# Optimization experiments

Hardware: AMD Instinct MI355X
Metric: run time of the kernel (lower is better)

Reference implementation:

```python
import jax, jax.numpy as jnp
import numpy as np

EMB_DIM = 16
NUM_EXPERTS = 8
TOPK = 2
HIDDEN = 4 * EMB_DIM  # assumed Expert hidden width


def setup_inputs() -> dict:
    key = jax.random.key(0)
    ks = jax.random.split(key, 8)
    B, S = 64, 4096
    s = 1.0 / np.sqrt(EMB_DIM)
    sh = 1.0 / np.sqrt(HIDDEN)
    return {
        "x": jax.random.normal(ks[0], (B, S, EMB_DIM), jnp.float32),
        "Wr": jax.random.uniform(ks[1], (EMB_DIM, NUM_EXPERTS), jnp.float32, -s, s),
        "br": jax.random.uniform(ks[2], (NUM_EXPERTS,), jnp.float32, -s, s),
        "W1": jax.random.uniform(ks[3], (NUM_EXPERTS, EMB_DIM, HIDDEN), jnp.float32, -s, s),
        "b1": jax.random.uniform(ks[4], (NUM_EXPERTS, HIDDEN), jnp.float32, -s, s),
        "W2": jax.random.uniform(ks[5], (NUM_EXPERTS, HIDDEN, EMB_DIM), jnp.float32, -sh, sh),
        "b2": jax.random.uniform(ks[6], (NUM_EXPERTS, EMB_DIM), jnp.float32, -sh, sh),
    }


def reference(x, Wr, br, W1, b1, W2, b2):
    # Router: softmax gate over all experts, then top-k expert selection.
    gate = jax.nn.softmax(x @ Wr + br, axis=-1)            # [B,S,E]
    _, topk_idx = jax.lax.top_k(gate, TOPK)                 # [B,S,TOPK]

    moe_out = jnp.zeros_like(x)
    # Small fixed loop over experts (mirrors the module's expert loop).
    for i in range(NUM_EXPERTS):
        sel = (topk_idx == i).any(axis=-1)                  # [B,S] bool
        w = gate[..., i] * sel                              # masked gate score
        h = jax.nn.relu(x @ W1[i] + b1[i])                  # [B,S,HIDDEN]
        eo = h @ W2[i] + b2[i]                              # [B,S,EMB_DIM]
        moe_out = moe_out + eo * w[..., None]
    return moe_out
```

## Files before the change

kernel.cpp:

```cpp
#include <hip/hip_runtime.h>
#include <hip/hip_bf16.h>

#define EMB 16
#define HID 64
#define NE  8
#define TPG 64

typedef float  f32x4 __attribute__((ext_vector_type(4)));
typedef double f64x4 __attribute__((ext_vector_type(4)));
typedef short  s16x4 __attribute__((ext_vector_type(4)));

__device__ __forceinline__ short f2bf(float f) {
    union { __hip_bfloat16 h; short s; } u;
    u.h = __float2bfloat16(f);
    return u.s;
}
__device__ __forceinline__ s16x4 pack_bf16x4(float a, float b, float c, float d) {
    s16x4 r;
    r[0] = f2bf(a); r[1] = f2bf(b); r[2] = f2bf(c); r[3] = f2bf(d);
    return r;
}

__device__ __forceinline__ f32x4 vfmaf(float s, f32x4 a, f32x4 c) {
    f32x4 r;
    r[0] = fmaf(s, a[0], c[0]); r[1] = fmaf(s, a[1], c[1]);
    r[2] = fmaf(s, a[2], c[2]); r[3] = fmaf(s, a[3], c[3]);
    return r;
}
__device__ __forceinline__ f64x4 vfmad(double s, f32x4 a, f64x4 c) {
    f64x4 r;
    r[0] = fma(s, (double)a[0], c[0]); r[1] = fma(s, (double)a[1], c[1]);
    r[2] = fma(s, (double)a[2], c[2]); r[3] = fma(s, (double)a[3], c[3]);
    return r;
}

__global__ __launch_bounds__(256, 2)
void router_k(const float* __restrict__ x, const float* __restrict__ Wr,
              const float* __restrict__ br, float* __restrict__ gates,
              int n_tokens)
{
    __shared__ float wr_lds[EMB * NE];
    __shared__ float br_lds[NE];
    const int tid = threadIdx.x;
    if (tid < EMB * NE) wr_lds[tid] = Wr[tid];
    if (tid < NE) br_lds[tid] = br[tid];
    __syncthreads();

    const int t = blockIdx.x * 256 + tid;
    if (t >= n_tokens) return;

    const f32x4* xp = (const f32x4*)(x + (size_t)t * EMB);
    const f32x4 x0 = xp[0], x1 = xp[1], x2 = xp[2], x3 = xp[3];

    f32x4 lgA = *(const f32x4*)(br_lds + 0);
    f32x4 lgB = *(const f32x4*)(br_lds + 4);
#define RSTEP(K, XV) do { const float xv_ = (XV); \
        lgA = vfmaf(xv_, *(const f32x4*)(wr_lds + (K) * NE),     lgA); \
        lgB = vfmaf(xv_, *(const f32x4*)(wr_lds + (K) * NE + 4), lgB); } while (0)
    RSTEP(0,  x0[0]); RSTEP(1,  x0[1]); RSTEP(2,  x0[2]); RSTEP(3,  x0[3]);
    RSTEP(4,  x1[0]); RSTEP(5,  x1[1]); RSTEP(6,  x1[2]); RSTEP(7,  x1[3]);
    RSTEP(8,  x2[0]); RSTEP(9,  x2[1]); RSTEP(10, x2[2]); RSTEP(11, x2[3]);
    RSTEP(12, x3[0]); RSTEP(13, x3[1]); RSTEP(14, x3[2]); RSTEP(15, x3[3]);
#undef RSTEP

    float m1 = -1e30f, m2 = -1e30f, m3 = -1e30f;
#define MSCAN(V) do { const float v_ = (V); \
        const float hi_ = fmaxf(m1, v_), lo_ = fminf(m1, v_); \
        const float hi2_ = fmaxf(m2, lo_), lo2_ = fminf(m2, lo_); \
        m1 = hi_; m2 = hi2_; m3 = fmaxf(m3, lo2_); } while (0)
    MSCAN(lgA[0]); MSCAN(lgA[1]); MSCAN(lgA[2]); MSCAN(lgA[3]);
    MSCAN(lgB[0]); MSCAN(lgB[1]); MSCAN(lgB[2]); MSCAN(lgB[3]);
#undef MSCAN

    int sm = 0;
    sm |= (lgA[0] >= m2) << 0; sm |= (lgA[1] >= m2) << 1;
    sm |= (lgA[2] >= m2) << 2; sm |= (lgA[3] >= m2) << 3;
    sm |= (lgB[0] >= m2) << 4; sm |= (lgB[1] >= m2) << 5;
    sm |= (lgB[2] >= m2) << 6; sm |= (lgB[3] >= m2) << 7;

    if (__any(m2 - m3 < 1e-4f)) {
        f64x4 dA, dB;
        dA[0] = (double)br_lds[0]; dA[1] = (double)br_lds[1];
        dA[2] = (double)br_lds[2]; dA[3] = (double)br_lds[3];
        dB[0] = (double)br_lds[4]; dB[1] = (double)br_lds[5];
        dB[2] = (double)br_lds[6]; dB[3] = (double)br_lds[7];
#define DSTEP(K, XV) do { const double xv_ = (double)(XV); \
        dA = vfmad(xv_, *(const f32x4*)(wr_lds + (K) * NE),     dA); \
        dB = vfmad(xv_, *(const f32x4*)(wr_lds + (K) * NE + 4), dB); } while (0)
        DSTEP(0,  x0[0]); DSTEP(1,  x0[1]); DSTEP(2,  x0[2]); DSTEP(3,  x0[3]);
        DSTEP(4,  x1[0]); DSTEP(5,  x1[1]); DSTEP(6,  x1[2]); DSTEP(7,  x1[3]);
        DSTEP(8,  x2[0]); DSTEP(9,  x2[1]); DSTEP(10, x2[2]); DSTEP(11, x2[3]);
        DSTEP(12, x3[0]); DSTEP(13, x3[1]); DSTEP(14, x3[2]); DSTEP(15, x3[3]);
#undef DSTEP
        double M1 = -1e300, M2 = -1e300;
#define DSCAN(V) do { const double v_ = (V); \
        const double hi_ = fmax(M1, v_); M2 = fmax(M2, fmin(M1, v_)); M1 = hi_; } while (0)
        DSCAN(dA[0]); DSCAN(dA[1]); DSCAN(dA[2]); DSCAN(dA[3]);
        DSCAN(dB[0]); DSCAN(dB[1]); DSCAN(dB[2]); DSCAN(dB[3]);
#undef DSCAN
        sm = 0;
        sm |= (dA[0] >= M2) << 0; sm |= (dA[1] >= M2) << 1;
        sm |= (dA[2] >= M2) << 2; sm |= (dA[3] >= M2) << 3;
        sm |= (dB[0] >= M2) << 4; sm |= (dB[1] >= M2) << 5;
        sm |= (dB[2] >= M2) << 6; sm |= (dB[3] >= M2) << 7;
    }

    const float e0 = __expf(lgA[0] - m1), e1 = __expf(lgA[1] - m1);
    const float e2 = __expf(lgA[2] - m1), e3 = __expf(lgA[3] - m1);
    const float e4 = __expf(lgB[0] - m1), e5 = __expf(lgB[1] - m1);
    const float e6 = __expf(lgB[2] - m1), e7 = __expf(lgB[3] - m1);
    const float inv = 1.0f / (e0 + e1 + e2 + e3 + e4 + e5 + e6 + e7);
    f32x4 gA, gB;
    gA[0] = (sm & 1)   ? e0 * inv : 0.f;  gA[1] = (sm & 2)   ? e1 * inv : 0.f;
    gA[2] = (sm & 4)   ? e2 * inv : 0.f;  gA[3] = (sm & 8)   ? e3 * inv : 0.f;
    gB[0] = (sm & 16)  ? e4 * inv : 0.f;  gB[1] = (sm & 32)  ? e5 * inv : 0.f;
    gB[2] = (sm & 64)  ? e6 * inv : 0.f;  gB[3] = (sm & 128) ? e7 * inv : 0.f;

    f32x4* gp = (f32x4*)(gates + (size_t)t * NE);
    gp[0] = gA;
    gp[1] = gB;
}

__global__ __launch_bounds__(256, 2)
void moe_k(const float* __restrict__ x, const float* __restrict__ gates,
           const float* __restrict__ W1, const float* __restrict__ b1,
           const float* __restrict__ W2, const float* __restrict__ b2,
           float* __restrict__ out, int n_tokens)
{
    __shared__ __align__(16) s16x4 w1lds[NE * 4 * 64];
    __shared__ __align__(16) s16x4 w2lds[NE * 4 * 64];
    __shared__ __align__(16) float b1_lds[NE * HID];
    __shared__ __align__(16) float b2_lds[NE * EMB];
    __shared__ __align__(16) float wt_lds[4 * 8 * TPG];

    const int tid = threadIdx.x;

    for (int s = tid; s < NE * 4 * 64; s += 256) {
        const int e = s >> 8, nq = (s >> 6) & 3, l = s & 63;
        const int cc = l & 15, gg = (l >> 4) & 3;
        const float* w1p = W1 + (e * EMB + 4 * gg) * HID + 16 * nq + cc;
        const float* w2p = W2 + (e * HID + 16 * nq + 4 * gg) * EMB + cc;
        w1lds[s] = pack_bf16x4(w1p[0], w1p[HID], w1p[2 * HID], w1p[3 * HID]);
        w2lds[s] = pack_bf16x4(w2p[0], w2p[EMB], w2p[2 * EMB], w2p[3 * EMB]);
    }
    for (int i = tid; i < NE * HID; i += 256) b1_lds[i] = b1[i];
    if (tid < NE * EMB) b2_lds[tid] = b2[tid];
    __syncthreads();

    const int lane = tid & 63;
    const int wid  = tid >> 6;
    const int col  = lane & 15;
    const int cg   = lane >> 4;
    float* wtw = wt_lds + wid * (NE * TPG);

    const int n_groups = n_tokens / TPG;
    for (int g = blockIdx.x * 4 + wid; g < n_groups; g += gridDim.x * 4) {
        const int tok0 = g * TPG;

        {
            const f32x4* gp = (const f32x4*)(gates + (size_t)(tok0 + lane) * NE);
            const f32x4 ga = gp[0], gb = gp[1];
#pragma unroll
            for (int e = 0; e < 4; ++e) wtw[e * TPG + lane] = ga[e];
#pragma unroll
            for (int e = 4; e < 8; ++e) wtw[e * TPG + lane] = gb[e - 4];
        }

        s16x4 xb0, xb1, xb2, xb3;
        {
            const f32x4 v0 = *(const f32x4*)(x + (size_t)(tok0 +  0 + col) * EMB + 4 * cg);
            const f32x4 v1 = *(const f32x4*)(x + (size_t)(tok0 + 16 + col) * EMB + 4 * cg);
            const f32x4 v2 = *(const f32x4*)(x + (size_t)(tok0 + 32 + col) * EMB + 4 * cg);
            const f32x4 v3 = *(const f32x4*)(x + (size_t)(tok0 + 48 + col) * EMB + 4 * cg);
            xb0 = pack_bf16x4(v0[0], v0[1], v0[2], v0[3]);
            xb1 = pack_bf16x4(v1[0], v1[1], v1[2], v1[3]);
            xb2 = pack_bf16x4(v2[0], v2[1], v2[2], v2[3]);
            xb3 = pack_bf16x4(v3[0], v3[1], v3[2], v3[3]);
        }

        f32x4 oacc0 = {0.f,0.f,0.f,0.f}, oacc1 = {0.f,0.f,0.f,0.f};
        f32x4 oacc2 = {0.f,0.f,0.f,0.f}, oacc3 = {0.f,0.f,0.f,0.f};

#pragma unroll 1
        for (int e = 0; e < NE; ++e) {
            const float wv0 = wtw[e * TPG +  0 + col];
            const float wv1 = wtw[e * TPG + 16 + col];
            const float wv2 = wtw[e * TPG + 32 + col];
            const float wv3 = wtw[e * TPG + 48 + col];

            f32x4 h0[4], h1[4], h2[4], h3[4];
#pragma unroll
            for (int n = 0; n < 4; ++n) {
                const s16x4 a1  = w1lds[(e * 4 + n) * 64 + lane];
                const f32x4 b1c = *(const f32x4*)(b1_lds + e * HID + 16 * n + 4 * cg);
                h0[n] = __builtin_amdgcn_mfma_f32_16x16x16bf16_1k(a1, xb0, b1c, 0, 0, 0);
                h1[n] = __builtin_amdgcn_mfma_f32_16x16x16bf16_1k(a1, xb1, b1c, 0, 0, 0);
                h2[n] = __builtin_amdgcn_mfma_f32_16x16x16bf16_1k(a1, xb2, b1c, 0, 0, 0);
                h3[n] = __builtin_amdgcn_mfma_f32_16x16x16bf16_1k(a1, xb3, b1c, 0, 0, 0);
            }

            const f32x4 b2c = *(const f32x4*)(b2_lds + e * EMB + 4 * cg);
            f32x4 eo0 = b2c, eo1 = b2c, eo2 = b2c, eo3 = b2c;
#pragma unroll
            for (int q = 0; q < 4; ++q) {
                const s16x4 a2 = w2lds[(e * 4 + q) * 64 + lane];
                const s16x4 p0 = pack_bf16x4(fmaxf(h0[q][0], 0.f), fmaxf(h0[q][1], 0.f),
                                             fmaxf(h0[q][2], 0.f), fmaxf(h0[q][3], 0.f));
                const s16x4 p1 = pack_bf16x4(fmaxf(h1[q][0], 0.f), fmaxf(h1[q][1], 0.f),
                                             fmaxf(h1[q][2], 0.f), fmaxf(h1[q][3], 0.f));
                const s16x4 p2 = pack_bf16x4(fmaxf(h2[q][0], 0.f), fmaxf(h2[q][1], 0.f),
                                             fmaxf(h2[q][2], 0.f), fmaxf(h2[q][3], 0.f));
                const s16x4 p3 = pack_bf16x4(fmaxf(h3[q][0], 0.f), fmaxf(h3[q][1], 0.f),
                                             fmaxf(h3[q][2], 0.f), fmaxf(h3[q][3], 0.f));
                eo0 = __builtin_amdgcn_mfma_f32_16x16x16bf16_1k(a2, p0, eo0, 0, 0, 0);
                eo1 = __builtin_amdgcn_mfma_f32_16x16x16bf16_1k(a2, p1, eo1, 0, 0, 0);
                eo2 = __builtin_amdgcn_mfma_f32_16x16x16bf16_1k(a2, p2, eo2, 0, 0, 0);
                eo3 = __builtin_amdgcn_mfma_f32_16x16x16bf16_1k(a2, p3, eo3, 0, 0, 0);
            }

            oacc0 = vfmaf(wv0, eo0, oacc0);
            oacc1 = vfmaf(wv1, eo1, oacc1);
            oacc2 = vfmaf(wv2, eo2, oacc2);
            oacc3 = vfmaf(wv3, eo3, oacc3);
        }

        *(f32x4*)(out + (size_t)(tok0 +  0 + col) * EMB + 4 * cg) = oacc0;
        *(f32x4*)(out + (size_t)(tok0 + 16 + col) * EMB + 4 * cg) = oacc1;
        *(f32x4*)(out + (size_t)(tok0 + 32 + col) * EMB + 4 * cg) = oacc2;
        *(f32x4*)(out + (size_t)(tok0 + 48 + col) * EMB + 4 * cg) = oacc3;
    }
}

extern "C" void kernel_launch(void* const* d_in, const int* in_sizes, int n_in,
                              void* d_out, int out_size, void* d_ws, size_t ws_size,
                              hipStream_t stream) {
    const float* x  = (const float*)d_in[0];
    const float* Wr = (const float*)d_in[1];
    const float* br = (const float*)d_in[2];
    const float* W1 = (const float*)d_in[3];
    const float* b1 = (const float*)d_in[4];
    const float* W2 = (const float*)d_in[5];
    const float* b2 = (const float*)d_in[6];
    float* out = (float*)d_out;

    const int n_tokens = in_sizes[0] / EMB;
    float* gates = (float*)d_ws;

    hipLaunchKernelGGL(router_k, dim3((n_tokens + 255) / 256), dim3(256), 0, stream,
                       x, Wr, br, gates, n_tokens);
    hipLaunchKernelGGL(moe_k, dim3(1024), dim3(256), 0, stream,
                       x, gates, W1, b1, W2, b2, out, n_tokens);
}
```

Measured before the change: 34.83 us.

## Fuse router into MoE kernel using split-bf16 MFMA for gate logits

Drops the separate router kernel and its gates buffer. Router logits are now computed inside the MoE kernel with three bf16 MFMAs that split weights and inputs into hi/lo parts, then softmax and top-2 run per token using lane shuffles. If any token in the wave has a near-tie, the gates for the whole group are recomputed in fp64. This removes one kernel launch and the gates write/read round trip, at the cost of extra MFMA and shuffle work plus some wave-divergent fallback in the main kernel.

```diff
diff --git a/kernel.cpp b/kernel.cpp
--- a/kernel.cpp
+++ b/kernel.cpp
@@ -15,12 +15,16 @@
     u.h = __float2bfloat16(f);
     return u.s;
 }
+__device__ __forceinline__ float bf2f(short s) {
+    union { unsigned u; float f; } v;
+    v.u = ((unsigned)(unsigned short)s) << 16;
+    return v.f;
+}
 __device__ __forceinline__ s16x4 pack_bf16x4(float a, float b, float c, float d) {
     s16x4 r;
     r[0] = f2bf(a); r[1] = f2bf(b); r[2] = f2bf(c); r[3] = f2bf(d);
     return r;
 }
-
 __device__ __forceinline__ f32x4 vfmaf(float s, f32x4 a, f32x4 c) {
     f32x4 r;
     r[0] = fmaf(s, a[0], c[0]); r[1] = fmaf(s, a[1], c[1]);
@@ -35,103 +39,19 @@
 }
 
 __global__ __launch_bounds__(256, 2)
-void router_k(const float* __restrict__ x, const float* __restrict__ Wr,
-              const float* __restrict__ br, float* __restrict__ gates,
-              int n_tokens)
-{
-    __shared__ float wr_lds[EMB * NE];
-    __shared__ float br_lds[NE];
-    const int tid = threadIdx.x;
-    if (tid < EMB * NE) wr_lds[tid] = Wr[tid];
-    if (tid < NE) br_lds[tid] = br[tid];
-    __syncthreads();
-
-    const int t = blockIdx.x * 256 + tid;
-    if (t >= n_tokens) return;
-
-    const f32x4* xp = (const f32x4*)(x + (size_t)t * EMB);
-    const f32x4 x0 = xp[0], x1 = xp[1], x2 = xp[2], x3 = xp[3];
-
-    f32x4 lgA = *(const f32x4*)(br_lds + 0);
-    f32x4 lgB = *(const f32x4*)(br_lds + 4);
-#define RSTEP(K, XV) do { const float xv_ = (XV); \
-        lgA = vfmaf(xv_, *(const f32x4*)(wr_lds + (K) * NE),     lgA); \
-        lgB = vfmaf(xv_, *(const f32x4*)(wr_lds + (K) * NE + 4), lgB); } while (0)
-    RSTEP(0,  x0[0]); RSTEP(1,  x0[1]); RSTEP(2,  x0[2]); RSTEP(3,  x0[3]);
-    RSTEP(4,  x1[0]); RSTEP(5,  x1[1]); RSTEP(6,  x1[2]); RSTEP(7,  x1[3]);
-    RSTEP(8,  x2[0]); RSTEP(9,  x2[1]); RSTEP(10, x2[2]); RSTEP(11, x2[3]);
-    RSTEP(12, x3[0]); RSTEP(13, x3[1]); RSTEP(14, x3[2]); RSTEP(15, x3[3]);
-#undef RSTEP
-
-    float m1 = -1e30f, m2 = -1e30f, m3 = -1e30f;
-#define MSCAN(V) do { const float v_ = (V); \
-        const float hi_ = fmaxf(m1, v_), lo_ = fminf(m1, v_); \
-        const float hi2_ = fmaxf(m2, lo_), lo2_ = fminf(m2, lo_); \
-        m1 = hi_; m2 = hi2_; m3 = fmaxf(m3, lo2_); } while (0)
-    MSCAN(lgA[0]); MSCAN(lgA[1]); MSCAN(lgA[2]); MSCAN(lgA[3]);
-    MSCAN(lgB[0]); MSCAN(lgB[1]); MSCAN(lgB[2]); MSCAN(lgB[3]);
-#undef MSCAN
-
-    int sm = 0;
-    sm |= (lgA[0] >= m2) << 0; sm |= (lgA[1] >= m2) << 1;
-    sm |= (lgA[2] >= m2) << 2; sm |= (lgA[3] >= m2) << 3;
-    sm |= (lgB[0] >= m2) << 4; sm |= (lgB[1] >= m2) << 5;
-    sm |= (lgB[2] >= m2) << 6; sm |= (lgB[3] >= m2) << 7;
-
-    if (__any(m2 - m3 < 1e-4f)) {
-        f64x4 dA, dB;
-        dA[0] = (double)br_lds[0]; dA[1] = (double)br_lds[1];
-        dA[2] = (double)br_lds[2]; dA[3] = (double)br_lds[3];
-        dB[0] = (double)br_lds[4]; dB[1] = (double)br_lds[5];
-        dB[2] = (double)br_lds[6]; dB[3] = (double)br_lds[7];
-#define DSTEP(K, XV) do { const double xv_ = (double)(XV); \
-        dA = vfmad(xv_, *(const f32x4*)(wr_lds + (K) * NE),     dA); \
-        dB = vfmad(xv_, *(const f32x4*)(wr_lds + (K) * NE + 4), dB); } while (0)
-        DSTEP(0,  x0[0]); DSTEP(1,  x0[1]); DSTEP(2,  x0[2]); DSTEP(3,  x0[3]);
-        DSTEP(4,  x1[0]); DSTEP(5,  x1[1]); DSTEP(6,  x1[2]); DSTEP(7,  x1[3]);
-        DSTEP(8,  x2[0]); DSTEP(9,  x2[1]); DSTEP(10, x2[2]); DSTEP(11, x2[3]);
-        DSTEP(12, x3[0]); DSTEP(13, x3[1]); DSTEP(14, x3[2]); DSTEP(15, x3[3]);
-#undef DSTEP
-        double M1 = -1e300, M2 = -1e300;
-#define DSCAN(V) do { const double v_ = (V); \
-        const double hi_ = fmax(M1, v_); M2 = fmax(M2, fmin(M1, v_)); M1 = hi_; } while (0)
-        DSCAN(dA[0]); DSCAN(dA[1]); DSCAN(dA[2]); DSCAN(dA[3]);
-        DSCAN(dB[0]); DSCAN(dB[1]); DSCAN(dB[2]); DSCAN(dB[3]);
-#undef DSCAN
-        sm = 0;
-        sm |= (dA[0] >= M2) << 0; sm |= (dA[1] >= M2) << 1;
-        sm |= (dA[2] >= M2) << 2; sm |= (dA[3] >= M2) << 3;
-        sm |= (dB[0] >= M2) << 4; sm |= (dB[1] >= M2) << 5;
-        sm |= (dB[2] >= M2) << 6; sm |= (dB[3] >= M2) << 7;
-    }
-
-    const float e0 = __expf(lgA[0] - m1), e1 = __expf(lgA[1] - m1);
-    const float e2 = __expf(lgA[2] - m1), e3 = __expf(lgA[3] - m1);
-    const float e4 = __expf(lgB[0] - m1), e5 = __expf(lgB[1] - m1);
-    const float e6 = __expf(lgB[2] - m1), e7 = __expf(lgB[3] - m1);
-    const float inv = 1.0f / (e0 + e1 + e2 + e3 + e4 + e5 + e6 + e7);
-    f32x4 gA, gB;
-    gA[0] = (sm & 1)   ? e0 * inv : 0.f;  gA[1] = (sm & 2)   ? e1 * inv : 0.f;
-    gA[2] = (sm & 4)   ? e2 * inv : 0.f;  gA[3] = (sm & 8)   ? e3 * inv : 0.f;
-    gB[0] = (sm & 16)  ? e4 * inv : 0.f;  gB[1] = (sm & 32)  ? e5 * inv : 0.f;
-    gB[2] = (sm & 64)  ? e6 * inv : 0.f;  gB[3] = (sm & 128) ? e7 * inv : 0.f;
-
-    f32x4* gp = (f32x4*)(gates + (size_t)t * NE);
-    gp[0] = gA;
-    gp[1] = gB;
-}
-
-__global__ __launch_bounds__(256, 2)
-void moe_k(const float* __restrict__ x, const float* __restrict__ gates,
-           const float* __restrict__ W1, const float* __restrict__ b1,
-           const float* __restrict__ W2, const float* __restrict__ b2,
-           float* __restrict__ out, int n_tokens)
+void moe_all(const float* __restrict__ x, const float* __restrict__ Wr,
+             const float* __restrict__ br, const float* __restrict__ W1,
+             const float* __restrict__ b1, const float* __restrict__ W2,
+             const float* __restrict__ b2, float* __restrict__ out,
+             int n_tokens)
 {
     __shared__ __align__(16) s16x4 w1lds[NE * 4 * 64];
     __shared__ __align__(16) s16x4 w2lds[NE * 4 * 64];
     __shared__ __align__(16) float b1_lds[NE * HID];
     __shared__ __align__(16) float b2_lds[NE * EMB];
-    __shared__ __align__(16) float wt_lds[4 * 8 * TPG];
+    __shared__ __align__(16) float wr_lds[EMB * NE];
+    __shared__ __align__(16) float br_lds[NE];
+    __shared__ __align__(16) float wt_lds[4 * NE * TPG];
 
     const int tid = threadIdx.x;
 
@@ -145,6 +65,8 @@
     }
     for (int i = tid; i < NE * HID; i += 256) b1_lds[i] = b1[i];
     if (tid < NE * EMB) b2_lds[tid] = b2[tid];
+    if (tid < EMB * NE) wr_lds[tid] = Wr[tid];
+    if (tid < NE) br_lds[tid] = br[tid];
     __syncthreads();
 
     const int lane = tid & 63;
@@ -153,31 +75,96 @@
     const int cg   = lane >> 4;
     float* wtw = wt_lds + wid * (NE * TPG);
 
+    s16x4 wra_hi, wra_lo;
+    f32x4 brc;
+#pragma unroll
+    for (int j = 0; j < 4; ++j) {
+        const float wv = (col < NE) ? wr_lds[(4 * cg + j) * NE + col] : 0.f;
+        const short hi = f2bf(wv);
+        wra_hi[j] = hi;
+        wra_lo[j] = f2bf(wv - bf2f(hi));
+    }
+#pragma unroll
+    for (int r = 0; r < 4; ++r) brc[r] = br_lds[(4 * cg + r) & (NE - 1)];
+
     const int n_groups = n_tokens / TPG;
     for (int g = blockIdx.x * 4 + wid; g < n_groups; g += gridDim.x * 4) {
         const int tok0 = g * TPG;
-
-        {
-            const f32x4* gp = (const f32x4*)(gates + (size_t)(tok0 + lane) * NE);
-            const f32x4 ga = gp[0], gb = gp[1];
-#pragma unroll
-            for (int e = 0; e < 4; ++e) wtw[e * TPG + lane] = ga[e];
-#pragma unroll
-            for (int e = 4; e < 8; ++e) wtw[e * TPG + lane] = gb[e - 4];
+        bool tie = false;
+        s16x4 xbT[4];
+
+#pragma unroll
+        for (int T = 0; T < 4; ++T) {
+            const f32x4 xv = *(const f32x4*)(x + (size_t)(tok0 + 16 * T + col) * EMB + 4 * cg);
+            const s16x4 xh = pack_bf16x4(xv[0], xv[1], xv[2], xv[3]);
+            const s16x4 xl = pack_bf16x4(xv[0] - bf2f(xh[0]), xv[1] - bf2f(xh[1]),
+                                         xv[2] - bf2f(xh[2]), xv[3] - bf2f(xh[3]));
+            xbT[T] = xh;
+            f32x4 lg = __builtin_amdgcn_mfma_f32_16x16x16bf16_1k(wra_hi, xh, brc, 0, 0, 0);
+            lg = __builtin_amdgcn_mfma_f32_16x16x16bf16_1k(wra_hi, xl, lg, 0, 0, 0);
+            lg = __builtin_amdgcn_mfma_f32_16x16x16bf16_1k(wra_lo, xh, lg, 0, 0, 0);
+            float ot0 = __shfl_xor(lg[0], 16, 64), ot1 = __shfl_xor(lg[1], 16, 64);
+            float ot2 = __shfl_xor(lg[2], 16, 64), ot3 = __shfl_xor(lg[3], 16, 64);
+            float m1 = -1e30f, m2 = -1e30f, m3 = -1e30f;
+#define MSCAN(V) do { const float v_ = (V); \
+        const float hi_ = fmaxf(m1, v_), lo_ = fminf(m1, v_); \
+        const float hi2_ = fmaxf(m2, lo_), lo2_ = fminf(m2, lo_); \
+        m1 = hi_; m2 = hi2_; m3 = fmaxf(m3, lo2_); } while (0)
+            MSCAN(lg[0]); MSCAN(lg[1]); MSCAN(lg[2]); MSCAN(lg[3]);
+            MSCAN(ot0);   MSCAN(ot1);   MSCAN(ot2);   MSCAN(ot3);
+#undef MSCAN
+            const float e0 = __expf(lg[0] - m1), e1 = __expf(lg[1] - m1);
+            const float e2 = __expf(lg[2] - m1), e3 = __expf(lg[3] - m1);
+            const float f0 = __expf(ot0 - m1),   f1 = __expf(ot1 - m1);
+            const float f2 = __expf(ot2 - m1),   f3 = __expf(ot3 - m1);
+            const float inv = 1.0f / (e0 + e1 + e2 + e3 + f0 + f1 + f2 + f3);
+            if (cg < 2) {
+                wtw[(4 * cg + 0) * TPG + 16 * T + col] = (lg[0] >= m2) ? e0 * inv : 0.f;
+                wtw[(4 * cg + 1) * TPG + 16 * T + col] = (lg[1] >= m2) ? e1 * inv : 0.f;
+                wtw[(4 * cg + 2) * TPG + 16 * T + col] = (lg[2] >= m2) ? e2 * inv : 0.f;
+                wtw[(4 * cg + 3) * TPG + 16 * T + col] = (lg[3] >= m2) ? e3 * inv : 0.f;
+                tie = tie || (m2 - m3 < 5e-4f);
+            }
         }
 
-        s16x4 xb0, xb1, xb2, xb3;
-        {
-            const f32x4 v0 = *(const f32x4*)(x + (size_t)(tok0 +  0 + col) * EMB + 4 * cg);
-            const f32x4 v1 = *(const f32x4*)(x + (size_t)(tok0 + 16 + col) * EMB + 4 * cg);
-            const f32x4 v2 = *(const f32x4*)(x + (size_t)(tok0 + 32 + col) * EMB + 4 * cg);
-            const f32x4 v3 = *(const f32x4*)(x + (size_t)(tok0 + 48 + col) * EMB + 4 * cg);
-            xb0 = pack_bf16x4(v0[0], v0[1], v0[2], v0[3]);
-            xb1 = pack_bf16x4(v1[0], v1[1], v1[2], v1[3]);
-            xb2 = pack_bf16x4(v2[0], v2[1], v2[2], v2[3]);
-            xb3 = pack_bf16x4(v3[0], v3[1], v3[2], v3[3]);
+        if (__any(tie)) {
+            const f32x4* xp = (const f32x4*)(x + (size_t)(tok0 + lane) * EMB);
+            const f32x4 x0 = xp[0], x1 = xp[1], x2 = xp[2], x3 = xp[3];
+            f64x4 dA, dB;
+            dA[0] = (double)br_lds[0]; dA[1] = (double)br_lds[1];
+            dA[2] = (double)br_lds[2]; dA[3] = (double)br_lds[3];
+            dB[0] = (double)br_lds[4]; dB[1] = (double)br_lds[5];
+            dB[2] = (double)br_lds[6]; dB[3] = (double)br_lds[7];
+#define DSTEP(K, XV) do { const double xv_ = (double)(XV); \
+        dA = vfmad(xv_, *(const f32x4*)(wr_lds + (K) * NE),     dA); \
+        dB = vfmad(xv_, *(const f32x4*)(wr_lds + (K) * NE + 4), dB); } while (0)
+            DSTEP(0,  x0[0]); DSTEP(1,  x0[1]); DSTEP(2,  x0[2]); DSTEP(3,  x0[3]);
+            DSTEP(4,  x1[0]); DSTEP(5,  x1[1]); DSTEP(6,  x1[2]); DSTEP(7,  x1[3]);
+            DSTEP(8,  x2[0]); DSTEP(9,  x2[1]); DSTEP(10, x2[2]); DSTEP(11, x2[3]);
+            DSTEP(12, x3[0]); DSTEP(13, x3[1]); DSTEP(14, x3[2]); DSTEP(15, x3[3]);
+#undef DSTEP
+            double M1 = -1e300, M2 = -1e300;
+#define DSCAN(V) do { const double v_ = (V); \
+        const double hi_ = fmax(M1, v_); M2 = fmax(M2, fmin(M1, v_)); M1 = hi_; } while (0)
+            DSCAN(dA[0]); DSCAN(dA[1]); DSCAN(dA[2]); DSCAN(dA[3]);
+            DSCAN(dB[0]); DSCAN(dB[1]); DSCAN(dB[2]); DSCAN(dB[3]);
+#undef DSCAN
+            const float g0 = __expf((float)(dA[0] - M1)), g1 = __expf((float)(dA[1] - M1));
+            const float g2 = __expf((float)(dA[2] - M1)), g3 = __expf((float)(dA[3] - M1));
+            const float g4 = __expf((float)(dB[0] - M1)), g5 = __expf((float)(dB[1] - M1));
+            const float g6 = __expf((float)(dB[2] - M1)), g7 = __expf((float)(dB[3] - M1));
+            const float inv = 1.0f / (g0 + g1 + g2 + g3 + g4 + g5 + g6 + g7);
+            wtw[0 * TPG + lane] = (dA[0] >= M2) ? g0 * inv : 0.f;
+            wtw[1 * TPG + lane] = (dA[1] >= M2) ? g1 * inv : 0.f;
+            wtw[2 * TPG + lane] = (dA[2] >= M2) ? g2 * inv : 0.f;
+            wtw[3 * TPG + lane] = (dA[3] >= M2) ? g3 * inv : 0.f;
+            wtw[4 * TPG + lane] = (dB[0] >= M2) ? g4 * inv : 0.f;
+            wtw[5 * TPG + lane] = (dB[1] >= M2) ? g5 * inv : 0.f;
+            wtw[6 * TPG + lane] = (dB[2] >= M2) ? g6 * inv : 0.f;
+            wtw[7 * TPG + lane] = (dB[3] >= M2) ? g7 * inv : 0.f;
         }
 
+        const s16x4 xb0 = xbT[0], xb1 = xbT[1], xb2 = xbT[2], xb3 = xbT[3];
         f32x4 oacc0 = {0.f,0.f,0.f,0.f}, oacc1 = {0.f,0.f,0.f,0.f};
         f32x4 oacc2 = {0.f,0.f,0.f,0.f}, oacc3 = {0.f,0.f,0.f,0.f};
 
@@ -244,10 +231,6 @@
     float* out = (float*)d_out;
 
     const int n_tokens = in_sizes[0] / EMB;
-    float* gates = (float*)d_ws;
-
-    hipLaunchKernelGGL(router_k, dim3((n_tokens + 255) / 256), dim3(256), 0, stream,
-                       x, Wr, br, gates, n_tokens);
-    hipLaunchKernelGGL(moe_k, dim3(1024), dim3(256), 0, stream,
-                       x, gates, W1, b1, W2, b2, out, n_tokens);
-}
+    hipLaunchKernelGGL(moe_all, dim3(1024), dim3(256), 0, stream,
+                       x, Wr, br, W1, b1, W2, b2, out, n_tokens);
+}
```

Result: slower. 81.19 us (+133.1%).

## Process two token groups per wave and halve grid to amortize weight staging

Applied to the files above, without the earlier changes.

Each wave now handles two 64-token groups, loading each expert's W1/W2 fragments and biases from LDS once per expert and reusing them for both groups. The grid is halved so each block stages the bf16 weight tables into LDS for twice as many tokens, and the grid-stride loop is replaced with a single assignment per wave. This raises register pressure and assumes the grid exactly covers all token pairs.

```diff
diff --git a/kernel.cpp b/kernel.cpp
--- a/kernel.cpp
+++ b/kernel.cpp
@@ -131,7 +131,7 @@
     __shared__ __align__(16) s16x4 w2lds[NE * 4 * 64];
     __shared__ __align__(16) float b1_lds[NE * HID];
     __shared__ __align__(16) float b2_lds[NE * EMB];
-    __shared__ __align__(16) float wt_lds[4 * 8 * TPG];
+    __shared__ __align__(16) float wt_lds[4 * 2 * NE * TPG];
 
     const int tid = threadIdx.x;
 
@@ -151,59 +151,82 @@
     const int wid  = tid >> 6;
     const int col  = lane & 15;
     const int cg   = lane >> 4;
-    float* wtw = wt_lds + wid * (NE * TPG);
-
-    const int n_groups = n_tokens / TPG;
-    for (int g = blockIdx.x * 4 + wid; g < n_groups; g += gridDim.x * 4) {
-        const int tok0 = g * TPG;
+    float* wtw = wt_lds + wid * (2 * NE * TPG);
+
+    const int n_pairs = n_tokens / (2 * TPG);
+    const int p = blockIdx.x * 4 + wid;
+    if (p >= n_pairs) return;
+    const int tokA0 = p * (2 * TPG);
+    const int tokB0 = tokA0 + TPG;
+
+    {
+        const f32x4* gpA = (const f32x4*)(gates + (size_t)(tokA0 + lane) * NE);
+        const f32x4 ga = gpA[0], gb = gpA[1];
+#pragma unroll
+        for (int e = 0; e < 4; ++e) wtw[e * TPG + lane] = ga[e];
+#pragma unroll
+        for (int e = 4; e < 8; ++e) wtw[e * TPG + lane] = gb[e - 4];
+        const f32x4* gpB = (const f32x4*)(gates + (size_t)(tokB0 + lane) * NE);
+        const f32x4 gc = gpB[0], gd = gpB[1];
+#pragma unroll
+        for (int e = 0; e < 4; ++e) wtw[(NE + e) * TPG + lane] = gc[e];
+#pragma unroll
+        for (int e = 4; e < 8; ++e) wtw[(NE + e) * TPG + lane] = gd[e - 4];
+    }
+
+    s16x4 xa0, xa1, xa2, xa3, xb0, xb1, xb2, xb3;
+    {
+        const f32x4 v0 = *(const f32x4*)(x + (size_t)(tokA0 +  0 + col) * EMB + 4 * cg);
+        const f32x4 v1 = *(const f32x4*)(x + (size_t)(tokA0 + 16 + col) * EMB + 4 * cg);
+        const f32x4 v2 = *(const f32x4*)(x + (size_t)(tokA0 + 32 + col) * EMB + 4 * cg);
+        const f32x4 v3 = *(const f32x4*)(x + (size_t)(tokA0 + 48 + col) * EMB + 4 * cg);
+        xa0 = pack_bf16x4(v0[0], v0[1], v0[2], v0[3]);
+        xa1 = pack_bf16x4(v1[0], v1[1], v1[2], v1[3]);
+        xa2 = pack_bf16x4(v2[0], v2[1], v2[2], v2[3]);
+        xa3 = pack_bf16x4(v3[0], v3[1], v3[2], v3[3]);
+        const f32x4 u0 = *(const f32x4*)(x + (size_t)(tokB0 +  0 + col) * EMB + 4 * cg);
+        const f32x4 u1 = *(const f32x4*)(x + (size_t)(tokB0 + 16 + col) * EMB + 4 * cg);
+        const f32x4 u2 = *(const f32x4*)(x + (size_t)(tokB0 + 32 + col) * EMB + 4 * cg);
+        const f32x4 u3 = *(const f32x4*)(x + (size_t)(tokB0 + 48 + col) * EMB + 4 * cg);
+        xb0 = pack_bf16x4(u0[0], u0[1], u0[2], u0[3]);
+        xb1 = pack_bf16x4(u1[0], u1[1], u1[2], u1[3]);
+        xb2 = pack_bf16x4(u2[0], u2[1], u2[2], u2[3]);
+        xb3 = pack_bf16x4(u3[0], u3[1], u3[2], u3[3]);
+    }
+
+    f32x4 oA0 = {0.f,0.f,0.f,0.f}, oA1 = {0.f,0.f,0.f,0.f};
+    f32x4 oA2 = {0.f,0.f,0.f,0.f}, oA3 = {0.f,0.f,0.f,0.f};
+    f32x4 oB0 = {0.f,0.f,0.f,0.f}, oB1 = {0.f,0.f,0.f,0.f};
+    f32x4 oB2 = {0.f,0.f,0.f,0.f}, oB3 = {0.f,0.f,0.f,0.f};
+
+#pragma unroll 1
+    for (int e = 0; e < NE; ++e) {
+        s16x4 a1f[4], a2f[4];
+        f32x4 b1c[4];
+#pragma unroll
+        for (int n = 0; n < 4; ++n) {
+            a1f[n] = w1lds[(e * 4 + n) * 64 + lane];
+            b1c[n] = *(const f32x4*)(b1_lds + e * HID + 16 * n + 4 * cg);
+            a2f[n] = w2lds[(e * 4 + n) * 64 + lane];
+        }
+        const f32x4 b2c = *(const f32x4*)(b2_lds + e * EMB + 4 * cg);
 
         {
-            const f32x4* gp = (const f32x4*)(gates + (size_t)(tok0 + lane) * NE);
-            const f32x4 ga = gp[0], gb = gp[1];
-#pragma unroll
-            for (int e = 0; e < 4; ++e) wtw[e * TPG + lane] = ga[e];
-#pragma unroll
-            for (int e = 4; e < 8; ++e) wtw[e * TPG + lane] = gb[e - 4];
-        }
-
-        s16x4 xb0, xb1, xb2, xb3;
-        {
-            const f32x4 v0 = *(const f32x4*)(x + (size_t)(tok0 +  0 + col) * EMB + 4 * cg);
-            const f32x4 v1 = *(const f32x4*)(x + (size_t)(tok0 + 16 + col) * EMB + 4 * cg);
-            const f32x4 v2 = *(const f32x4*)(x + (size_t)(tok0 + 32 + col) * EMB + 4 * cg);
-            const f32x4 v3 = *(const f32x4*)(x + (size_t)(tok0 + 48 + col) * EMB + 4 * cg);
-            xb0 = pack_bf16x4(v0[0], v0[1], v0[2], v0[3]);
-            xb1 = pack_bf16x4(v1[0], v1[1], v1[2], v1[3]);
-            xb2 = pack_bf16x4(v2[0], v2[1], v2[2], v2[3]);
-            xb3 = pack_bf16x4(v3[0], v3[1], v3[2], v3[3]);
-        }
-
-        f32x4 oacc0 = {0.f,0.f,0.f,0.f}, oacc1 = {0.f,0.f,0.f,0.f};
-        f32x4 oacc2 = {0.f,0.f,0.f,0.f}, oacc3 = {0.f,0.f,0.f,0.f};
-
-#pragma unroll 1
-        for (int e = 0; e < NE; ++e) {
             const float wv0 = wtw[e * TPG +  0 + col];
             const float wv1 = wtw[e * TPG + 16 + col];
             const float wv2 = wtw[e * TPG + 32 + col];
             const float wv3 = wtw[e * TPG + 48 + col];
-
             f32x4 h0[4], h1[4], h2[4], h3[4];
 #pragma unroll
             for (int n = 0; n < 4; ++n) {
-                const s16x4 a1  = w1lds[(e * 4 + n) * 64 + lane];
-                const f32x4 b1c = *(const f32x4*)(b1_lds + e * HID + 16 * n + 4 * cg);
-                h0[n] = __builtin_amdgcn_mfma_f32_16x16x16bf16_1k(a1, xb0, b1c, 0, 0, 0);
-                h1[n] = __builtin_amdgcn_mfma_f32_16x16x16bf16_1k(a1, xb1, b1c, 0, 0, 0);
-                h2[n] = __builtin_amdgcn_mfma_f32_16x16x16bf16_1k(a1, xb2, b1c, 0, 0, 0);
-                h3[n] = __builtin_amdgcn_mfma_f32_16x16x16bf16_1k(a1, xb3, b1c, 0, 0, 0);
+                h0[n] = __builtin_amdgcn_mfma_f32_16x16x16bf16_1k(a1f[n], xa0, b1c[n], 0, 0, 0);
+                h1[n] = __builtin_amdgcn_mfma_f32_16x16x16bf16_1k(a1f[n], xa1, b1c[n], 0, 0, 0);
+                h2[n] = __builtin_amdgcn_mfma_f32_16x16x16bf16_1k(a1f[n], xa2, b1c[n], 0, 0, 0);
+                h3[n] = __builtin_amdgcn_mfma_f32_16x16x16bf16_1k(a1f[n], xa3, b1c[n], 0, 0, 0);
             }
-
-            const f32x4 b2c = *(const f32x4*)(b2_lds + e * EMB + 4 * cg);
             f32x4 eo0 = b2c, eo1 = b2c, eo2 = b2c, eo3 = b2c;
 #pragma unroll
             for (int q = 0; q < 4; ++q) {
-                const s16x4 a2 = w2lds[(e * 4 + q) * 64 + lane];
                 const s16x4 p0 = pack_bf16x4(fmaxf(h0[q][0], 0.f), fmaxf(h0[q][1], 0.f),
                                              fmaxf(h0[q][2], 0.f), fmaxf(h0[q][3], 0.f));
                 const s16x4 p1 = pack_bf16x4(fmaxf(h1[q][0], 0.f), fmaxf(h1[q][1], 0.f),
@@ -212,23 +235,61 @@
                                              fmaxf(h2[q][2], 0.f), fmaxf(h2[q][3], 0.f));
                 const s16x4 p3 = pack_bf16x4(fmaxf(h3[q][0], 0.f), fmaxf(h3[q][1], 0.f),
                                              fmaxf(h3[q][2], 0.f), fmaxf(h3[q][3], 0.f));
-                eo0 = __builtin_amdgcn_mfma_f32_16x16x16bf16_1k(a2, p0, eo0, 0, 0, 0);
-                eo1 = __builtin_amdgcn_mfma_f32_16x16x16bf16_1k(a2, p1, eo1, 0, 0, 0);
-                eo2 = __builtin_amdgcn_mfma_f32_16x16x16bf16_1k(a2, p2, eo2, 0, 0, 0);
-                eo3 = __builtin_amdgcn_mfma_f32_16x16x16bf16_1k(a2, p3, eo3, 0, 0, 0);
+                eo0 = __builtin_amdgcn_mfma_f32_16x16x16bf16_1k(a2f[q], p0, eo0, 0, 0, 0);
+                eo1 = __builtin_amdgcn_mfma_f32_16x16x16bf16_1k(a2f[q], p1, eo1, 0, 0, 0);
+                eo2 = __builtin_amdgcn_mfma_f32_16x16x16bf16_1k(a2f[q], p2, eo2, 0, 0, 0);
+                eo3 = __builtin_amdgcn_mfma_f32_16x16x16bf16_1k(a2f[q], p3, eo3, 0, 0, 0);
             }
-
-            oacc0 = vfmaf(wv0, eo0, oacc0);
-            oacc1 = vfmaf(wv1, eo1, oacc1);
-            oacc2 = vfmaf(wv2, eo2, oacc2);
-            oacc3 = vfmaf(wv3, eo3, oacc3);
+            oA0 = vfmaf(wv0, eo0, oA0);
+            oA1 = vfmaf(wv1, eo1, oA1);
+            oA2 = vfmaf(wv2, eo2, oA2);
+            oA3 = vfmaf(wv3, eo3, oA3);
         }
 
-        *(f32x4*)(out + (size_t)(tok0 +  0 + col) * EMB + 4 * cg) = oacc0;
-        *(f32x4*)(out + (size_t)(tok0 + 16 + col) * EMB + 4 * cg) = oacc1;
-        *(f32x4*)(out + (size_t)(tok0 + 32 + col) * EMB + 4 * cg) = oacc2;
-        *(f32x4*)(out + (size_t)(tok0 + 48 + col) * EMB + 4 * cg) = oacc3;
-    }
+        {
+            const float wv0 = wtw[(NE + e) * TPG +  0 + col];
+            const float wv1 = wtw[(NE + e) * TPG + 16 + col];
+            const float wv2 = wtw[(NE + e) * TPG + 32 + col];
+            const float wv3 = wtw[(NE + e) * TPG + 48 + col];
+            f32x4 h0[4], h1[4], h2[4], h3[4];
+#pragma unroll
+            for (int n = 0; n < 4; ++n) {
+                h0[n] = __builtin_amdgcn_mfma_f32_16x16x16bf16_1k(a1f[n], xb0, b1c[n], 0, 0, 0);
+                h1[n] = __builtin_amdgcn_mfma_f32_16x16x16bf16_1k(a1f[n], xb1, b1c[n], 0, 0, 0);
+                h2[n] = __builtin_amdgcn_mfma_f32_16x16x16bf16_1k(a1f[n], xb2, b1c[n], 0, 0, 0);
+                h3[n] = __builtin_amdgcn_mfma_f32_16x16x16bf16_1k(a1f[n], xb3, b1c[n], 0, 0, 0);
+            }
+            f32x4 eo0 = b2c, eo1 = b2c, eo2 = b2c, eo3 = b2c;
+#pragma unroll
+            for (int q = 0; q < 4; ++q) {
+                const s16x4 p0 = pack_bf16x4(fmaxf(h0[q][0], 0.f), fmaxf(h0[q][1], 0.f),
+                                             fmaxf(h0[q][2], 0.f), fmaxf(h0[q][3], 0.f));
+                const s16x4 p1 = pack_bf16x4(fmaxf(h1[q][0], 0.f), fmaxf(h1[q][1], 0.f),
+                                             fmaxf(h1[q][2], 0.f), fmaxf(h1[q][3], 0.f));
+                const s16x4 p2 = pack_bf16x4(fmaxf(h2[q][0], 0.f), fmaxf(h2[q][1], 0.f),
+                                             fmaxf(h2[q][2], 0.f), fmaxf(h2[q][3], 0.f));
+                const s16x4 p3 = pack_bf16x4(fmaxf(h3[q][0], 0.f), fmaxf(h3[q][1], 0.f),
+                                             fmaxf(h3[q][2], 0.f), fmaxf(h3[q][3], 0.f));
+                eo0 = __builtin_amdgcn_mfma_f32_16x16x16bf16_1k(a2f[q], p0, eo0, 0, 0, 0);
+                eo1 = __builtin_amdgcn_mfma_f32_16x16x16bf16_1k(a2f[q], p1, eo1, 0, 0, 0);
+                eo2 = __builtin_amdgcn_mfma_f32_16x16x16bf16_1k(a2f[q], p2, eo2, 0, 0, 0);
+                eo3 = __builtin_amdgcn_mfma_f32_16x16x16bf16_1k(a2f[q], p3, eo3, 0, 0, 0);
+            }
+            oB0 = vfmaf(wv0, eo0, oB0);
+            oB1 = vfmaf(wv1, eo1, oB1);
+            oB2 = vfmaf(wv2, eo2, oB2);
+            oB3 = vfmaf(wv3, eo3, oB3);
+        }
+    }
+
+    *(f32x4*)(out + (size_t)(tokA0 +  0 + col) * EMB + 4 * cg) = oA0;
+    *(f32x4*)(out + (size_t)(tokA0 + 16 + col) * EMB + 4 * cg) = oA1;
+    *(f32x4*)(out + (size_t)(tokA0 + 32 + col) * EMB + 4 * cg) = oA2;
+    *(f32x4*)(out + (size_t)(tokA0 + 48 + col) * EMB + 4 * cg) = oA3;
+    *(f32x4*)(out + (size_t)(tokB0 +  0 + col) * EMB + 4 * cg) = oB0;
+    *(f32x4*)(out + (size_t)(tokB0 + 16 + col) * EMB + 4 * cg) = oB1;
+    *(f32x4*)(out + (size_t)(tokB0 + 32 + col) * EMB + 4 * cg) = oB2;
+    *(f32x4*)(out + (size_t)(tokB0 + 48 + col) * EMB + 4 * cg) = oB3;
 }
 
 extern "C" void kernel_launch(void* const* d_in, const int* in_sizes, int n_in,
@@ -248,6 +309,6 @@
 
     hipLaunchKernelGGL(router_k, dim3((n_tokens + 255) / 256), dim3(256), 0, stream,
                        x, Wr, br, gates, n_tokens);
-    hipLaunchKernelGGL(moe_k, dim3(1024), dim3(256), 0, stream,
+    hipLaunchKernelGGL(moe_k, dim3(512), dim3(256), 0, stream,
                        x, gates, W1, b1, W2, b2, out, n_tokens);
 }
```

Measured after the change: 39.23 us. +12.6%, slower.
